# Kernel tuning notes

Hardware: AMD Instinct MI355X
Metric: run time of the kernel (lower is better)

## Reference

```python
import jax, jax.numpy as jnp
import numpy as np
from jax import lax

B, C_IN, T = 256, 1, 1632
HID, CB_DIM, NUM_TOK, NUM_Q = 64, 512, 1024, 2


def conv_k2s2(x, W, b):
    # Conv1d(kernel=2, stride=2): x [B,Ci,T] -> [B,Co,T//2]; W [Co,Ci,2]
    Bx, Ci, Tx = x.shape
    xr = x.reshape(Bx, Ci, Tx // 2, 2)
    return jnp.einsum('bitk,oik->bot', xr, W) + b[None, :, None]


def convT_k2s2(x, W, b):
    # ConvTranspose1d(kernel=2, stride=2): x [B,Ci,T] -> [B,Co,2T]; W [Ci,Co,2] (torch layout)
    Bx, Ci, Tx = x.shape
    y = jnp.einsum('bit,iok->botk', x, W)  # [B,Co,T,2]
    Co = W.shape[1]
    return y.reshape(Bx, Co, 2 * Tx) + b[None, :, None]


def conv1x1(x, W, b):
    # W [Co,Ci]
    return jnp.einsum('bit,oi->bot', x, W) + b[None, :, None]


def residual_vq(x, codebooks):
    # x [B,t,D]; codebooks [NUM_Q, NUM_TOK, D]. Euclidean argmin + straight-through.
    residual = x
    quantized_out = jnp.zeros_like(x)
    all_idx, all_loss = [], []
    for q in range(codebooks.shape[0]):
        cb = codebooks[q]  # [N,D]
        # squared euclidean distance, single large GEMM
        d2 = (jnp.sum(residual ** 2, -1, keepdims=True)
              - 2.0 * jnp.einsum('btd,nd->btn', residual, cb)
              + jnp.sum(cb ** 2, -1))  # [B,t,N]
        idx = jnp.argmin(d2, axis=-1)  # [B,t]
        quant = cb[idx]  # gather [B,t,D]
        # commitment loss (codebook treated as fixed / EMA-updated)
        loss = jnp.mean((lax.stop_gradient(quant) - residual) ** 2)
        # straight-through estimator
        quant_st = residual + lax.stop_gradient(quant - residual)
        residual = residual - lax.stop_gradient(quant)
        quantized_out = quantized_out + quant_st
        all_idx.append(idx)
        all_loss.append(loss)
    return quantized_out, jnp.stack(all_idx, -1), jnp.stack(all_loss)


def setup_inputs() -> dict:
    key = jax.random.key(0)
    ks = jax.random.split(key, 16)
    s = 0.02
    return {
        'img': jax.random.normal(ks[0], (B, C_IN, T), jnp.float32),
        'W_e1': jax.random.normal(ks[1], (HID, C_IN, 2), jnp.float32) * s,
        'b_e1': jnp.zeros((HID,), jnp.float32),
        'W_e2': jax.random.normal(ks[2], (HID, HID, 2), jnp.float32) * s,
        'b_e2': jnp.zeros((HID,), jnp.float32),
        'W_e3': jax.random.normal(ks[3], (CB_DIM, HID), jnp.float32) * s,
        'b_e3': jnp.zeros((CB_DIM,), jnp.float32),
        'codebooks': jax.random.normal(ks[4], (NUM_Q, NUM_TOK, CB_DIM), jnp.float32),
        'Wt_d1': jax.random.normal(ks[5], (CB_DIM, HID, 2), jnp.float32) * s,
        'b_d1': jnp.zeros((HID,), jnp.float32),
        'Wt_d2': jax.random.normal(ks[6], (HID, HID, 2), jnp.float32) * s,
        'b_d2': jnp.zeros((HID,), jnp.float32),
        'W_d3': jax.random.normal(ks[7], (C_IN, HID), jnp.float32) * s,
        'b_d3': jnp.zeros((C_IN,), jnp.float32),
    }


def reference(img, W_e1, b_e1, W_e2, b_e2, W_e3, b_e3, codebooks,
              Wt_d1, b_d1, Wt_d2, b_d2, W_d3, b_d3):
    # encoder
    h = jax.nn.relu(conv_k2s2(img, W_e1, b_e1))
    h = jax.nn.relu(conv_k2s2(h, W_e2, b_e2))
    encoded = conv1x1(h, W_e3, b_e3)  # [B,512,408]
    # residual VQ over tokens
    x = jnp.transpose(encoded, (0, 2, 1))  # b c t -> b t c
    quantized, indices, commit_loss = residual_vq(x, codebooks)
    quantized = jnp.transpose(quantized, (0, 2, 1))  # b t c -> b c t
    # decoder
    d = jax.nn.relu(convT_k2s2(quantized, Wt_d1, b_d1))
    d = jax.nn.relu(convT_k2s2(d, Wt_d2, b_d2))
    out = conv1x1(d, W_d3, b_d3)  # [B,1,1632]
    recon_loss = jnp.mean((img - out) ** 2)
    return out, recon_loss, commit_loss, indices, quantized
```

## Files before the change

### kernel.cpp

```cpp
#include <hip/hip_runtime.h>

#define NB    256
#define TLEN  1632
#define HIDC  64
#define CBD   512
#define NTOK  1024
#define T2L   816
#define T4L   408
#define MTOK  (NB*T4L)
#define M2TOK (NB*T2L)
#define MOUT  (NB*TLEN)

#define DO_OUT    ((size_t)0)
#define DO_RECON  ((size_t)417792)
#define DO_IDX    ((size_t)417795)
#define DO_QUANT  ((size_t)626691)

typedef unsigned short u16;
typedef unsigned long long u64;
typedef __attribute__((ext_vector_type(8))) short short8;
typedef __attribute__((ext_vector_type(4))) float f32x4;
typedef __attribute__((ext_vector_type(8))) _Float16 half8;
typedef __attribute__((ext_vector_type(4))) _Float16 half4;

static constexpr size_t OFF_XR  = 0;
static constexpr size_t OFF_H1  = OFF_XR + (size_t)MTOK*512;
static constexpr size_t OFF_H2  = OFF_H1 + (size_t)NB*T2L*64;
static constexpr size_t OFF_BE2 = OFF_H2 + (size_t)NB*T4L*64;
static constexpr size_t OFF_BD1 = OFF_BE2 + 8192;
static constexpr size_t OFF_BD2 = OFF_BD1 + 65536;
static constexpr size_t OFF_BX1 = OFF_BD2 + 8192;
static constexpr size_t OFF_BX2 = OFF_BX1 + 128;
static constexpr size_t OFF_ZB  = OFF_BX2 + 128;
static constexpr size_t OFF_C2  = OFF_ZB + 128;
static constexpr size_t OFF_SLOT= OFF_C2 + 2048;
static constexpr size_t OFF_IDXI= OFF_SLOT + 1536;
static constexpr size_t OFF_KEYS= OFF_IDXI + (size_t)MTOK*2;
static constexpr size_t OFF_FC  = OFF_KEYS + (size_t)MTOK*4;
static constexpr size_t OFF_FLAG= OFF_FC + 4;
static constexpr size_t OFF_CBH = OFF_FLAG + (size_t)MTOK*2;
static constexpr size_t OFF_CBL = OFF_CBH + 524288;
static constexpr size_t OFF_P0  = OFF_CBL + 524288;
static constexpr size_t OFF_P1  = OFF_P0 + 131072;

__device__ inline u64 shfl_xor_u64_w16(u64 v, int m) {
    unsigned lo = (unsigned)v, hi = (unsigned)(v >> 32);
    lo = __shfl_xor(lo, m, 16);
    hi = __shfl_xor(hi, m, 16);
    return (((u64)hi) << 32) | lo;
}
__device__ inline u64 packkey(float d, int n) {
    unsigned u = __float_as_uint(d);
    u = (u & 0x80000000u) ? ~u : (u | 0x80000000u);
    return (((u64)u) << 32) | (unsigned)n;
}
__device__ inline float unpackd(u64 k) {
    unsigned u = (unsigned)(k >> 32);
    u = (u & 0x80000000u) ? (u & 0x7fffffffu) : ~u;
    return __uint_as_float(u);
}
__device__ inline void merge2(u64& k1, u64& k2, u64 o1, u64 o2) {
    u64 n1 = (k1 < o1) ? k1 : o1;
    u64 hi = (k1 < o1) ? o1 : k1;
    u64 cand = (k1 <= o1) ? k2 : o2;
    u64 n2 = (hi < cand) ? hi : cand;
    k1 = n1; k2 = n2;
}
__device__ inline half4 cvt_h4(float4 v) {
    half4 h;
    h.x = (_Float16)v.x; h.y = (_Float16)v.y;
    h.z = (_Float16)v.z; h.w = (_Float16)v.w;
    return h;
}
__device__ inline half8 cvt_h8(float4 v0, float4 v1) {
    half8 h;
    h[0] = (_Float16)v0.x; h[1] = (_Float16)v0.y;
    h[2] = (_Float16)v0.z; h[3] = (_Float16)v0.w;
    h[4] = (_Float16)v1.x; h[5] = (_Float16)v1.y;
    h[6] = (_Float16)v1.z; h[7] = (_Float16)v1.w;
    return h;
}

__global__ void setup_kernel(const float* __restrict__ We2, const float* __restrict__ Wtd1,
                             const float* __restrict__ Wtd2, const float* __restrict__ bd1,
                             const float* __restrict__ bd2, const float* __restrict__ cbs,
                             float* __restrict__ Be2, float* __restrict__ Bd1,
                             float* __restrict__ Bd2, float* __restrict__ bx1, float* __restrict__ bx2,
                             u16* __restrict__ cbh, float* __restrict__ c2) {
    size_t t = (size_t)blockIdx.x * 256 + threadIdx.x;
    {
        float4 v = *(const float4*)(cbs + t * 4);
        *(half4*)&cbh[t * 4] = cvt_h4(v);
    }
    {
        int w = (int)(t >> 6);
        int lane = threadIdx.x & 63;
        if (w < 2048) {
            const float* r = cbs + (size_t)w * 512;
            float4 a = *(const float4*)(r + lane * 8);
            float4 b = *(const float4*)(r + lane * 8 + 4);
            float s = a.x*a.x + a.y*a.y + a.z*a.z + a.w*a.w + b.x*b.x + b.y*b.y + b.z*b.z + b.w*b.w;
            #pragma unroll
            for (int o = 32; o > 0; o >>= 1) s += __shfl_down(s, o, 64);
            if (lane == 0) c2[w] = s;
        }
    }
    size_t stride = (size_t)gridDim.x * 256;
    for (size_t x = t; x < 64 * 128; x += stride) {
        int c = (int)(x >> 7), k = (int)(x & 127);
        Be2[x] = We2[c * 128 + ((k & 63) << 1) + (k >> 6)];
    }
    for (size_t x = t; x < 128 * 512; x += stride) {
        int n = (int)(x >> 9), k = (int)(x & 511);
        Bd1[x] = Wtd1[k * 128 + n];
    }
    for (size_t x = t; x < 128 * 64; x += stride) {
        int n = (int)(x >> 6), k = (int)(x & 63);
        Bd2[x] = Wtd2[k * 128 + n];
    }
    for (size_t x = t; x < 128; x += stride) { bx1[x] = bd1[x >> 1]; bx2[x] = bd2[x >> 1]; }
}

__global__ void enc1_kernel(const float* __restrict__ img, const float* __restrict__ W,
                            const float* __restrict__ bias, float* __restrict__ h1) {
    int idx = blockIdx.x * 256 + threadIdx.x;
    int c = idx & 63;
    int t = (idx >> 6) % T2L;
    int b = idx / (64 * T2L);
    float v = W[c * 2] * img[(size_t)b * TLEN + 2 * t] +
              W[c * 2 + 1] * img[(size_t)b * TLEN + 2 * t + 1] + bias[c];
    h1[idx] = fmaxf(v, 0.f);
}

__global__ __launch_bounds__(256) void gemm_nt(const float* __restrict__ A, const float* __restrict__ Bw,
                        const float* __restrict__ bias, float* __restrict__ C,
                        int M, int N, int K, int amode, int relu) {
    __shared__ float As[32][132];
    __shared__ float Bs[32][68];
    int m0 = blockIdx.x * 128;
    int n0 = blockIdx.y * 64;
    int tid = threadIdx.x;
    int tx = tid & 15;
    int ty = tid >> 4;
    float acc[8][4];
    #pragma unroll
    for (int i = 0; i < 8; ++i)
        #pragma unroll
        for (int j = 0; j < 4; ++j) acc[i][j] = 0.f;

    for (int k0 = 0; k0 < K; k0 += 32) {
        #pragma unroll
        for (int i = 0; i < 4; ++i) {
            int idx = tid + i * 256;
            int row = idx >> 3;
            int kq = idx & 7;
            int m = m0 + row;
            size_t base;
            if (amode == 0) base = (size_t)m * K;
            else            base = (size_t)(((m / T4L) * T2L + 2 * (m % T4L)) * 64);
            float4 v = *(const float4*)(A + base + k0 + kq * 4);
            int kk = kq * 4;
            As[kk + 0][row] = v.x; As[kk + 1][row] = v.y;
            As[kk + 2][row] = v.z; As[kk + 3][row] = v.w;
        }
        #pragma unroll
        for (int i = 0; i < 2; ++i) {
            int idx = tid + i * 256;
            int row = idx >> 3;
            int kq = idx & 7;
            float4 v = *(const float4*)(Bw + (size_t)(n0 + row) * K + k0 + kq * 4);
            int kk = kq * 4;
            Bs[kk + 0][row] = v.x; Bs[kk + 1][row] = v.y;
            Bs[kk + 2][row] = v.z; Bs[kk + 3][row] = v.w;
        }
        __syncthreads();
        #pragma unroll
        for (int kk = 0; kk < 32; ++kk) {
            float a[8], bf[4];
            float4 a0 = *(const float4*)&As[kk][ty * 8];
            float4 a1 = *(const float4*)&As[kk][ty * 8 + 4];
            a[0]=a0.x; a[1]=a0.y; a[2]=a0.z; a[3]=a0.w;
            a[4]=a1.x; a[5]=a1.y; a[6]=a1.z; a[7]=a1.w;
            float4 b0 = *(const float4*)&Bs[kk][tx * 4];
            bf[0]=b0.x; bf[1]=b0.y; bf[2]=b0.z; bf[3]=b0.w;
            #pragma unroll
            for (int i = 0; i < 8; ++i)
                #pragma unroll
                for (int j = 0; j < 4; ++j) acc[i][j] += a[i] * bf[j];
        }
        __syncthreads();
    }
    #pragma unroll
    for (int i = 0; i < 8; ++i) {
        int m = m0 + ty * 8 + i;
        float4 v;
        v.x = acc[i][0] + bias[n0 + tx * 4 + 0];
        v.y = acc[i][1] + bias[n0 + tx * 4 + 1];
        v.z = acc[i][2] + bias[n0 + tx * 4 + 2];
        v.w = acc[i][3] + bias[n0 + tx * 4 + 3];
        if (relu) { v.x=fmaxf(v.x,0.f); v.y=fmaxf(v.y,0.f); v.z=fmaxf(v.z,0.f); v.w=fmaxf(v.w,0.f); }
        *(float4*)(C + (size_t)m * N + n0 + tx * 4) = v;
    }
}

template<int Q1>
__global__ __launch_bounds__(256, 3) void vq_f16_db(
    const float* __restrict__ Ap, const u16* __restrict__ cbh,
    const float* __restrict__ c2, const u64* __restrict__ prevkeys,
    const u16* __restrict__ cb0h, u64* __restrict__ pairs)
{
    __shared__ __align__(16) u16 As[2][128 * 40];
    __shared__ __align__(16) u16 Bs[2][128 * 40];
    int tid = threadIdx.x;
    int n0 = blockIdx.x * 128, m0 = blockIdx.y * 128;
    int lane = tid & 63, wid = tid >> 6;
    int lm = lane & 15, quad = lane >> 4;
    int wm = wid >> 1, wn = wid & 1;

    f32x4 acc[4][4];
    #pragma unroll
    for (int i = 0; i < 4; ++i)
        #pragma unroll
        for (int j = 0; j < 4; ++j) acc[i][j] = (f32x4){0.f, 0.f, 0.f, 0.f};

    int rw[2], cq[2];
    size_t coff[2];
    #pragma unroll
    for (int i = 0; i < 2; ++i) {
        int idx = tid + i * 256;
        rw[i] = idx >> 2; cq[i] = idx & 3;
        if (Q1) {
            int i0 = (int)(prevkeys[m0 + rw[i]] & 0xFFFFFFFFull);
            coff[i] = (size_t)i0 * 512;
        }
    }

#define VQ_LOAD(K0, AV0, AV1, CH, BV)                                                 \
    _Pragma("unroll")                                                                 \
    for (int i = 0; i < 2; ++i) {                                                     \
        AV0[i] = *(const float4*)(Ap + (size_t)(m0 + rw[i]) * 512 + (K0) + cq[i]*8);  \
        AV1[i] = *(const float4*)(Ap + (size_t)(m0 + rw[i]) * 512 + (K0) + cq[i]*8 + 4);\
        if (Q1) CH[i] = *(const half8*)(cb0h + coff[i] + (K0) + cq[i]*8);             \
        BV[i] = *(const short8*)(cbh + (size_t)(n0 + rw[i]) * 512 + (K0) + cq[i]*8);  \
    }

#define VQ_WRITE(BUF, AV0, AV1, CH, BV)                                               \
    _Pragma("unroll")                                                                 \
    for (int i = 0; i < 2; ++i) {                                                     \
        half8 hv = cvt_h8(AV0[i], AV1[i]);                                            \
        if (Q1) hv = hv - CH[i];                                                      \
        *(half8*)&As[BUF][rw[i] * 40 + cq[i] * 8] = hv;                               \
        *(short8*)&Bs[BUF][rw[i] * 40 + cq[i] * 8] = BV[i];                           \
    }

#define VQ_COMPUTE(BUF) {                                                             \
        half8 ah[4];                                                                  \
        _Pragma("unroll")                                                             \
        for (int mt = 0; mt < 4; ++mt)                                                \
            ah[mt] = *(const half8*)&As[BUF][(wm*64 + mt*16 + lm) * 40 + quad * 8];   \
        _Pragma("unroll")                                                             \
        for (int nt = 0; nt < 4; ++nt) {                                              \
            half8 bh = *(const half8*)&Bs[BUF][(wn*64 + nt*16 + lm) * 40 + quad * 8]; \
            _Pragma("unroll")                                                         \
            for (int mt = 0; mt < 4; ++mt)                                            \
                acc[mt][nt] = __builtin_amdgcn_mfma_f32_16x16x32_f16(ah[mt], bh, acc[mt][nt], 0, 0, 0); \
        }                                                                             \
    }

    float4 a0A[2], a1A[2], a0B[2], a1B[2];
    half8 chA[2], chB[2];
    short8 bvA[2], bvB[2];
    (void)chA; (void)chB;

    VQ_LOAD(0, a0A, a1A, chA, bvA);
    VQ_WRITE(0, a0A, a1A, chA, bvA);
    VQ_LOAD(32, a0B, a1B, chB, bvB);
    __syncthreads();

    for (int tp = 0; tp < 8; ++tp) {
        {
            VQ_WRITE(1, a0B, a1B, chB, bvB);
            if (tp < 7) { int K0 = (2 * tp + 2) * 32; VQ_LOAD(K0, a0A, a1A, chA, bvA); }
            VQ_COMPUTE(0);
            __syncthreads();
        }
        {
            if (tp < 7) { VQ_WRITE(0, a0A, a1A, chA, bvA); }
            if (tp < 7) { int K0 = (2 * tp + 3) * 32; VQ_LOAD(K0, a0B, a1B, chB, bvB); }
            VQ_COMPUTE(1);
            __syncthreads();
        }
    }
#undef VQ_LOAD
#undef VQ_WRITE
#undef VQ_COMPUTE

    float c2v[4];
    #pragma unroll
    for (int nt = 0; nt < 4; ++nt) c2v[nt] = c2[n0 + wn * 64 + nt * 16 + lm];

    u64* scr = (u64*)&As[0][0];
    #pragma unroll
    for (int mt = 0; mt < 4; ++mt) {
        #pragma unroll
        for (int rg = 0; rg < 4; ++rg) {
            int tl = wm * 64 + mt * 16 + quad * 4 + rg;
            u64 k1 = ~0ull, k2 = ~0ull;
            #pragma unroll
            for (int nt = 0; nt < 4; ++nt) {
                float d = c2v[nt] - 2.0f * acc[mt][nt][rg];
                u64 k = packkey(d, n0 + wn * 64 + nt * 16 + lm);
                if (k < k1) { k2 = k1; k1 = k; } else if (k < k2) { k2 = k; }
            }
            #pragma unroll
            for (int s = 1; s < 16; s <<= 1) {
                u64 o1 = shfl_xor_u64_w16(k1, s);
                u64 o2 = shfl_xor_u64_w16(k2, s);
                merge2(k1, k2, o1, o2);
            }
            if (lm == 0) { scr[wn * 256 + tl * 2] = k1; scr[wn * 256 + tl * 2 + 1] = k2; }
        }
    }
    __syncthreads();
    if (tid < 128) {
        u64 a1 = scr[tid * 2], a2 = scr[tid * 2 + 1];
        merge2(a1, a2, scr[256 + tid * 2], scr[256 + tid * 2 + 1]);
        size_t base = (size_t)(m0 + tid) * 16 + blockIdx.x * 2;
        pairs[base] = a1; pairs[base + 1] = a2;
    }
}

__global__ void vq_reduce(const u64* __restrict__ pairs, u64* __restrict__ keybuf,
                          int* __restrict__ fc, int* __restrict__ flaglist, float tau) {
    int m = blockIdx.x * 256 + threadIdx.x;
    const u64* p = pairs + (size_t)m * 16;
    u64 k1 = ~0ull, k2 = ~0ull;
    #pragma unroll
    for (int i = 0; i < 16; ++i) {
        u64 k = p[i];
        if (k < k1) { k2 = k1; k1 = k; } else if (k < k2) { k2 = k; }
    }
    keybuf[m] = k1;
    if (unpackd(k2) - unpackd(k1) < tau) {
        int pos = atomicAdd(fc, 1);
        flaglist[pos] = m;
    }
}

__global__ void vq_rescue(const float* __restrict__ xr, const float* __restrict__ cb,
                          const float* __restrict__ c2, const float* __restrict__ cb0,
                          const u64* __restrict__ prevkeys,
                          const int* __restrict__ fc, const int* __restrict__ flaglist,
                          u64* __restrict__ keybuf) {
    __shared__ u64 red[4];
    int cnt = *fc;
    int lane = threadIdx.x & 63, wid = threadIdx.x >> 6;
    for (int f = blockIdx.x; f < cnt; f += gridDim.x) {
        int m = flaglist[f];
        float4 rv0 = *(const float4*)(xr + (size_t)m * 512 + lane * 8);
        float4 rv1 = *(const float4*)(xr + (size_t)m * 512 + lane * 8 + 4);
        if (cb0) {
            size_t co = (size_t)(prevkeys[m] & 0xFFFFFFFFull) * 512;
            float4 c0 = *(const float4*)(cb0 + co + lane * 8);
            float4 c1 = *(const float4*)(cb0 + co + lane * 8 + 4);
            rv0.x -= c0.x; rv0.y -= c0.y; rv0.z -= c0.z; rv0.w -= c0.w;
            rv1.x -= c1.x; rv1.y -= c1.y; rv1.z -= c1.z; rv1.w -= c1.w;
        }
        u64 best = ~0ull;
        for (int c = wid * 256; c < wid * 256 + 256; ++c) {
            const float* cp = cb + (size_t)c * 512 + lane * 8;
            float4 c0 = *(const float4*)cp;
            float4 c1 = *(const float4*)(cp + 4);
            float p = rv0.x*c0.x + rv0.y*c0.y + rv0.z*c0.z + rv0.w*c0.w
                    + rv1.x*c1.x + rv1.y*c1.y + rv1.z*c1.z + rv1.w*c1.w;
            #pragma unroll
            for (int s = 1; s < 64; s <<= 1) p += __shfl_xor(p, s, 64);
            u64 k = packkey(c2[c] - 2.0f * p, c);
            if (k < best) best = k;
        }
        if (lane == 0) red[wid] = best;
        __syncthreads();
        if (threadIdx.x == 0) {
            u64 b = red[0];
            if (red[1] < b) b = red[1];
            if (red[2] < b) b = red[2];
            if (red[3] < b) b = red[3];
            keybuf[m] = b;
        }
        __syncthreads();
    }
}

__global__ void commit_idx_kernel(const float* __restrict__ xr,
                                  const float* __restrict__ cb0f, const float* __restrict__ cb1f,
                                  const u64* __restrict__ keys0, const u64* __restrict__ keys1,
                                  float* __restrict__ idx_f, int* __restrict__ idx_i,
                                  float* __restrict__ slots) {
    int tid = threadIdx.x;
    int lane = tid & 63;
    int m = blockIdx.x * 4 + (tid >> 6);
    unsigned i0 = (unsigned)(keys0[m] & 0xFFFFFFFFull);
    unsigned i1 = (unsigned)(keys1[m] & 0xFFFFFFFFull);
    const float* x = xr + (size_t)m * 512 + lane * 8;
    const float* c0 = cb0f + (size_t)i0 * 512 + lane * 8;
    const float* c1 = cb1f + (size_t)i1 * 512 + lane * 8;
    float4 x0 = *(const float4*)x, x1 = *(const float4*)(x + 4);
    float4 a0 = *(const float4*)c0, a1 = *(const float4*)(c0 + 4);
    float4 b0 = *(const float4*)c1, b1 = *(const float4*)(c1 + 4);
    x0.x -= a0.x; x0.y -= a0.y; x0.z -= a0.z; x0.w -= a0.w;
    x1.x -= a1.x; x1.y -= a1.y; x1.z -= a1.z; x1.w -= a1.w;
    float s1 = x0.x*x0.x + x0.y*x0.y + x0.z*x0.z + x0.w*x0.w
             + x1.x*x1.x + x1.y*x1.y + x1.z*x1.z + x1.w*x1.w;
    x0.x -= b0.x; x0.y -= b0.y; x0.z -= b0.z; x0.w -= b0.w;
    x1.x -= b1.x; x1.y -= b1.y; x1.z -= b1.z; x1.w -= b1.w;
    float s2 = x0.x*x0.x + x0.y*x0.y + x0.z*x0.z + x0.w*x0.w
             + x1.x*x1.x + x1.y*x1.y + x1.z*x1.z + x1.w*x1.w;
    #pragma unroll
    for (int o = 32; o > 0; o >>= 1) { s1 += __shfl_down(s1, o, 64); s2 += __shfl_down(s2, o, 64); }
    if (lane == 0) {
        atomicAdd(&slots[512 + (m & 511)], s1);
        atomicAdd(&slots[1024 + (m & 511)], s2);
        idx_f[(size_t)m * 2]     = (float)i0;
        idx_f[(size_t)m * 2 + 1] = (float)i1;
        idx_i[m * 2] = (int)i0;
        idx_i[m * 2 + 1] = (int)i1;
    }
}

__global__ void quant_out_kernel(const float* __restrict__ cb0, const float* __restrict__ cb1,
                                 const int* __restrict__ idxi, float* __restrict__ out4) {
    __shared__ float buf[64][129];
    __shared__ int i0s[64], i1s[64];
    int b = blockIdx.x;
    int t0 = blockIdx.y * 64;
    int c0 = blockIdx.z * 128;
    int tid = threadIdx.x;
    if (tid < 64) {
        int t = t0 + tid;
        int i0 = 0, i1 = 0;
        if (t < T4L) { i0 = idxi[(b * T4L + t) * 2]; i1 = idxi[(b * T4L + t) * 2 + 1]; }
        i0s[tid] = i0; i1s[tid] = i1;
    }
    __syncthreads();
    int cl = tid & 127, th = tid >> 7;
    for (int t = th; t < 64; t += 2) {
        if (t0 + t < T4L)
            buf[t][cl] = cb0[(size_t)i0s[t] * 512 + c0 + cl] + cb1[(size_t)i1s[t] * 512 + c0 + cl];
    }
    __syncthreads();
    int lane = tid & 63, ch = tid >> 6;
    for (int cc = ch; cc < 128; cc += 4) {
        int t = t0 + lane;
        if (t < T4L) out4[((size_t)b * 512 + c0 + cc) * T4L + t] = buf[lane][cc];
    }
}

__global__ void d1_gather_kernel(const float* __restrict__ P0, const float* __restrict__ P1,
                                 const int* __restrict__ idxi, const float* __restrict__ bx1,
                                 float* __restrict__ d1) {
    int x = blockIdx.x * 256 + threadIdx.x;
    int n = x & 127;
    int m = x >> 7;
    int b = m / T4L, t = m % T4L;
    int i0 = idxi[m * 2], i1 = idxi[m * 2 + 1];
    float v = P0[i0 * 128 + n] + P1[i1 * 128 + n] + bx1[n];
    v = fmaxf(v, 0.f);
    d1[((size_t)(b * T2L + 2 * t + (n & 1))) * 64 + (n >> 1)] = v;
}

__global__ __launch_bounds__(256) void dec2_fused(
    const float* __restrict__ d1, const float* __restrict__ Bd2, const float* __restrict__ bx2,
    const float* __restrict__ W3, const float* __restrict__ b3, const float* __restrict__ img,
    float* __restrict__ out, float* __restrict__ slots)
{
    __shared__ float As[32][132];
    __shared__ float Bs[32][132];
    __shared__ float w3s[64];
    int m0 = blockIdx.x * 128;
    int tid = threadIdx.x;
    int tx = tid & 15;
    int ty = tid >> 4;
    if (tid < 64) w3s[tid] = W3[tid];
    float acc[8][8];
    #pragma unroll
    for (int i = 0; i < 8; ++i)
        #pragma unroll
        for (int j = 0; j < 8; ++j) acc[i][j] = 0.f;

    for (int k0 = 0; k0 < 64; k0 += 32) {
        #pragma unroll
        for (int i = 0; i < 4; ++i) {
            int idx = tid + i * 256;
            int row = idx >> 3;
            int kq = idx & 7;
            float4 v = *(const float4*)(d1 + (size_t)(m0 + row) * 64 + k0 + kq * 4);
            int kk = kq * 4;
            As[kk + 0][row] = v.x; As[kk + 1][row] = v.y;
            As[kk + 2][row] = v.z; As[kk + 3][row] = v.w;
        }
        #pragma unroll
        for (int i = 0; i < 4; ++i) {
            int idx = tid + i * 256;
            int row = idx >> 3;
            int kq = idx & 7;
            float4 v = *(const float4*)(Bd2 + (size_t)row * 64 + k0 + kq * 4);
            int kk = kq * 4;
            Bs[kk + 0][row] = v.x; Bs[kk + 1][row] = v.y;
            Bs[kk + 2][row] = v.z; Bs[kk + 3][row] = v.w;
        }
        __syncthreads();
        #pragma unroll
        for (int kk = 0; kk < 32; ++kk) {
            float a[8], bf[8];
            float4 a0 = *(const float4*)&As[kk][ty * 8];
            float4 a1 = *(const float4*)&As[kk][ty * 8 + 4];
            a[0]=a0.x; a[1]=a0.y; a[2]=a0.z; a[3]=a0.w;
            a[4]=a1.x; a[5]=a1.y; a[6]=a1.z; a[7]=a1.w;
            float4 b0 = *(const float4*)&Bs[kk][tx * 4];
            float4 b1 = *(const float4*)&Bs[kk][64 + tx * 4];
            bf[0]=b0.x; bf[1]=b0.y; bf[2]=b0.z; bf[3]=b0.w;
            bf[4]=b1.x; bf[5]=b1.y; bf[6]=b1.z; bf[7]=b1.w;
            #pragma unroll
            for (int i = 0; i < 8; ++i)
                #pragma unroll
                for (int j = 0; j < 8; ++j) acc[i][j] += a[i] * bf[j];
        }
        __syncthreads();
    }
    float bb3 = b3[0];
    float local = 0.f;
    #pragma unroll
    for (int i = 0; i < 8; ++i) {
        float s0 = 0.f, s1 = 0.f;
        #pragma unroll
        for (int j = 0; j < 4; ++j) {
            int n = tx * 4 + j;
            float v = fmaxf(acc[i][j] + bx2[n], 0.f);
            float w = w3s[n >> 1];
            if (j & 1) s1 += w * v; else s0 += w * v;
            int n2 = 64 + tx * 4 + j;
            float v2 = fmaxf(acc[i][j + 4] + bx2[n2], 0.f);
            float w2 = w3s[n2 >> 1];
            if (j & 1) s1 += w2 * v2; else s0 += w2 * v2;
        }
        #pragma unroll
        for (int o = 8; o > 0; o >>= 1) { s0 += __shfl_down(s0, o, 16); s1 += __shfl_down(s1, o, 16); }
        if (tx == 0) {
            int m = m0 + ty * 8 + i;
            int b = m / T2L, t2 = m % T2L;
            size_t o0 = (size_t)b * TLEN + 2 * t2;
            float v0 = s0 + bb3, v1 = s1 + bb3;
            out[o0] = v0; out[o0 + 1] = v1;
            float e0 = img[o0] - v0, e1 = img[o0 + 1] - v1;
            local += e0 * e0 + e1 * e1;
        }
    }
    if (tx == 0) atomicAdd(&slots[(blockIdx.x * 16 + ty) & 511], local);
}

__global__ void finalize_kernel(const float* __restrict__ slots, float* __restrict__ out_scalars) {
    __shared__ float red[256];
    int tid = threadIdx.x;
    for (int which = 0; which < 3; ++which) {
        float s = slots[which * 512 + tid] + slots[which * 512 + tid + 256];
        red[tid] = s; __syncthreads();
        for (int st = 128; st > 0; st >>= 1) { if (tid < st) red[tid] += red[tid + st]; __syncthreads(); }
        if (tid == 0) {
            float denom = (which == 0) ? (float)MOUT : (float)((size_t)MTOK * 512);
            out_scalars[which] = red[0] / denom;
        }
        __syncthreads();
    }
}

extern "C" void kernel_launch(void* const* d_in, const int* in_sizes, int n_in,
                              void* d_out, int out_size, void* d_ws, size_t ws_size,
                              hipStream_t stream) {
    const float* img  = (const float*)d_in[0];
    const float* We1  = (const float*)d_in[1];
    const float* be1  = (const float*)d_in[2];
    const float* We2  = (const float*)d_in[3];
    const float* be2  = (const float*)d_in[4];
    const float* We3  = (const float*)d_in[5];
    const float* be3  = (const float*)d_in[6];
    const float* cbs  = (const float*)d_in[7];
    const float* Wtd1 = (const float*)d_in[8];
    const float* bd1  = (const float*)d_in[9];
    const float* Wtd2 = (const float*)d_in[10];
    const float* bd2  = (const float*)d_in[11];
    const float* Wd3  = (const float*)d_in[12];
    const float* bd3  = (const float*)d_in[13];

    float* w = (float*)d_ws;
    float* xr   = w + OFF_XR;
    float* h1   = w + OFF_H1;
    float* h2   = w + OFF_H2;
    float* Be2  = w + OFF_BE2;
    float* Bd1  = w + OFF_BD1;
    float* Bd2  = w + OFF_BD2;
    float* bx1  = w + OFF_BX1;
    float* bx2  = w + OFF_BX2;
    float* zerob= w + OFF_ZB;
    float* c2   = w + OFF_C2;
    float* slots= w + OFF_SLOT;
    int*   idxi = (int*)(w + OFF_IDXI);
    u64*   keys = (u64*)(w + OFF_KEYS);
    int*   fc   = (int*)(w + OFF_FC);
    int*   flag = (int*)(w + OFF_FLAG);
    u16*   cbh  = (u16*)(w + OFF_CBH);
    float* P0   = w + OFF_P0;
    float* P1   = w + OFF_P1;
    u64*   pairs= (u64*)(w + OFF_H2);

    float* outp = (float*)d_out;
    float* out0   = outp + DO_OUT;
    float* oscal  = outp + DO_RECON;
    float* idxf   = outp + DO_IDX;
    float* qout   = outp + DO_QUANT;

    hipMemsetAsync(slots, 0, 1536 * sizeof(float), stream);
    hipMemsetAsync(fc, 0, 2 * sizeof(int), stream);
    hipMemsetAsync(zerob, 0, 128 * sizeof(float), stream);

    setup_kernel<<<1024, 256, 0, stream>>>(We2, Wtd1, Wtd2, bd1, bd2, cbs,
                                           Be2, Bd1, Bd2, bx1, bx2, cbh, c2);

    const float* cb1p = cbs + (size_t)NTOK * CBD;

    gemm_nt<<<dim3(8, 2), 256, 0, stream>>>(cbs,  Bd1, zerob, P0, 1024, 128, 512, 0, 0);
    gemm_nt<<<dim3(8, 2), 256, 0, stream>>>(cb1p, Bd1, zerob, P1, 1024, 128, 512, 0, 0);

    enc1_kernel<<<(NB * T2L * HIDC) / 256, 256, 0, stream>>>(img, We1, be1, h1);
    gemm_nt<<<dim3(MTOK / 128, 1), 256, 0, stream>>>(h1, Be2, be2, h2, MTOK, 64, 128, 1, 1);
    gemm_nt<<<dim3(MTOK / 128, 8), 256, 0, stream>>>(h2, We3, be3, xr, MTOK, 512, 64, 0, 0);

    vq_f16_db<0><<<dim3(8, MTOK / 128), 256, 0, stream>>>(xr, cbh, c2, nullptr, nullptr, pairs);
    vq_reduce<<<MTOK / 256, 256, 0, stream>>>(pairs, keys, fc + 0, flag, 0.05f);
    vq_rescue<<<1024, 256, 0, stream>>>(xr, cbs, c2, nullptr, nullptr, fc + 0, flag, keys);
    vq_f16_db<1><<<dim3(8, MTOK / 128), 256, 0, stream>>>(xr, cbh + (size_t)NTOK * 512,
                                                          c2 + NTOK, keys, cbh, pairs);
    vq_reduce<<<MTOK / 256, 256, 0, stream>>>(pairs, keys + MTOK, fc + 1, flag + MTOK, 0.15f);
    vq_rescue<<<1024, 256, 0, stream>>>(xr, cb1p, c2 + NTOK, cbs, keys, fc + 1, flag + MTOK, keys + MTOK);

    commit_idx_kernel<<<MTOK / 4, 256, 0, stream>>>(xr, cbs, cb1p, keys, keys + MTOK, idxf, idxi, slots);

    quant_out_kernel<<<dim3(NB, 7, 4), 256, 0, stream>>>(cbs, cb1p, idxi, qout);

    d1_gather_kernel<<<(MTOK * 128) / 256, 256, 0, stream>>>(P0, P1, idxi, bx1, h1);
    dec2_fused<<<M2TOK / 128, 256, 0, stream>>>(h1, Bd2, bx2, Wd3, bd3, img, out0, slots);

    finalize_kernel<<<1, 256, 0, stream>>>(slots, oscal);
}
```

Measured before the change: 1.319 ms.

## Widen VQ distance GEMM tile to 256 codes with direct-to-LDS codebook loads

Each block of the VQ distance kernel now covers 256 codebook entries instead of 128. This halves the grid in N and halves how often each fp32 activation tile is reloaded and converted. The codebook tile is copied straight from global memory into LDS with global_load_lds, using an XOR-swizzled layout to avoid bank conflicts, which saves register staging. The pairs buffer moves to its own workspace region and the reduce reads 8 partial candidates per token instead of 16. The costs are twice the accumulator registers and occupancy dropping from 3 to 2 waves per SIMD.

```diff
diff --git a/kernel.cpp b/kernel.cpp
--- a/kernel.cpp
+++ b/kernel.cpp
@@ -42,6 +42,7 @@
 static constexpr size_t OFF_CBL = OFF_CBH + 524288;
 static constexpr size_t OFF_P0  = OFF_CBL + 524288;
 static constexpr size_t OFF_P1  = OFF_P0 + 131072;
+static constexpr size_t OFF_PAIRS = OFF_P1 + 131072;
 
 __device__ inline u64 shfl_xor_u64_w16(u64 v, int m) {
     unsigned lo = (unsigned)v, hi = (unsigned)(v >> 32);
@@ -79,6 +80,10 @@
     h[4] = (_Float16)v1.x; h[5] = (_Float16)v1.y;
     h[6] = (_Float16)v1.z; h[7] = (_Float16)v1.w;
     return h;
+}
+__device__ inline void gll16(const u16* g, u16* l) {
+    __builtin_amdgcn_global_load_lds((const __attribute__((address_space(1))) void*)g,
+                                     (__attribute__((address_space(3))) void*)l, 16, 0, 0);
 }
 
 __global__ void setup_kernel(const float* __restrict__ We2, const float* __restrict__ Wtd1,
@@ -204,53 +209,62 @@
 }
 
 template<int Q1>
-__global__ __launch_bounds__(256, 3) void vq_f16_db(
+__global__ __launch_bounds__(256, 2) void vq_f16_db(
     const float* __restrict__ Ap, const u16* __restrict__ cbh,
     const float* __restrict__ c2, const u64* __restrict__ prevkeys,
     const u16* __restrict__ cb0h, u64* __restrict__ pairs)
 {
     __shared__ __align__(16) u16 As[2][128 * 40];
-    __shared__ __align__(16) u16 Bs[2][128 * 40];
+    __shared__ __align__(16) u16 Bs[2][256 * 32];
     int tid = threadIdx.x;
-    int n0 = blockIdx.x * 128, m0 = blockIdx.y * 128;
+    int n0 = blockIdx.x * 256, m0 = blockIdx.y * 128;
     int lane = tid & 63, wid = tid >> 6;
     int lm = lane & 15, quad = lane >> 4;
     int wm = wid >> 1, wn = wid & 1;
 
-    f32x4 acc[4][4];
+    f32x4 acc[4][8];
     #pragma unroll
     for (int i = 0; i < 4; ++i)
         #pragma unroll
-        for (int j = 0; j < 4; ++j) acc[i][j] = (f32x4){0.f, 0.f, 0.f, 0.f};
-
-    int rw[2], cq[2];
-    size_t coff[2];
+        for (int j = 0; j < 8; ++j) acc[i][j] = (f32x4){0.f, 0.f, 0.f, 0.f};
+
+    int ar[2], acq[2], coffA[2];
     #pragma unroll
     for (int i = 0; i < 2; ++i) {
         int idx = tid + i * 256;
-        rw[i] = idx >> 2; cq[i] = idx & 3;
-        if (Q1) {
-            int i0 = (int)(prevkeys[m0 + rw[i]] & 0xFFFFFFFFull);
-            coff[i] = (size_t)i0 * 512;
-        }
-    }
-
-#define VQ_LOAD(K0, AV0, AV1, CH, BV)                                                 \
+        ar[i] = idx >> 2; acq[i] = idx & 3;
+        coffA[i] = 0;
+        if (Q1) coffA[i] = (int)(prevkeys[m0 + ar[i]] & 0xFFFFFFFFull) * 512;
+    }
+    int brow[4], bchk[4];
+    #pragma unroll
+    for (int i = 0; i < 4; ++i) {
+        brow[i] = i * 64 + wid * 16 + (lane >> 2);
+        bchk[i] = (lane & 3) ^ ((brow[i] >> 1) & 3);
+    }
+
+#define VQ_GLLB(BUF, K0)                                                              \
+    _Pragma("unroll")                                                                 \
+    for (int i = 0; i < 4; ++i) {                                                     \
+        const u16* gp = cbh + (size_t)(n0 + brow[i]) * 512 + (K0) + bchk[i] * 8;      \
+        gll16(gp, &Bs[BUF][i * 2048 + wid * 512]);                                    \
+    }
+
+#define VQ_LOADA(K0, V0, V1, CH)                                                      \
     _Pragma("unroll")                                                                 \
     for (int i = 0; i < 2; ++i) {                                                     \
-        AV0[i] = *(const float4*)(Ap + (size_t)(m0 + rw[i]) * 512 + (K0) + cq[i]*8);  \
-        AV1[i] = *(const float4*)(Ap + (size_t)(m0 + rw[i]) * 512 + (K0) + cq[i]*8 + 4);\
-        if (Q1) CH[i] = *(const half8*)(cb0h + coff[i] + (K0) + cq[i]*8);             \
-        BV[i] = *(const short8*)(cbh + (size_t)(n0 + rw[i]) * 512 + (K0) + cq[i]*8);  \
-    }
-
-#define VQ_WRITE(BUF, AV0, AV1, CH, BV)                                               \
+        const float* s = Ap + (size_t)(m0 + ar[i]) * 512 + (K0) + acq[i] * 8;         \
+        V0[i] = *(const float4*)s;                                                    \
+        V1[i] = *(const float4*)(s + 4);                                              \
+        if (Q1) CH[i] = *(const half8*)(cb0h + coffA[i] + (K0) + acq[i] * 8);         \
+    }
+
+#define VQ_WRITEA(BUF, V0, V1, CH)                                                    \
     _Pragma("unroll")                                                                 \
     for (int i = 0; i < 2; ++i) {                                                     \
-        half8 hv = cvt_h8(AV0[i], AV1[i]);                                            \
+        half8 hv = cvt_h8(V0[i], V1[i]);                                              \
         if (Q1) hv = hv - CH[i];                                                      \
-        *(half8*)&As[BUF][rw[i] * 40 + cq[i] * 8] = hv;                               \
-        *(short8*)&Bs[BUF][rw[i] * 40 + cq[i] * 8] = BV[i];                           \
+        *(half8*)&As[BUF][ar[i] * 40 + acq[i] * 8] = hv;                              \
     }
 
 #define VQ_COMPUTE(BUF) {                                                             \
@@ -259,45 +273,51 @@
         for (int mt = 0; mt < 4; ++mt)                                                \
             ah[mt] = *(const half8*)&As[BUF][(wm*64 + mt*16 + lm) * 40 + quad * 8];   \
         _Pragma("unroll")                                                             \
-        for (int nt = 0; nt < 4; ++nt) {                                              \
-            half8 bh = *(const half8*)&Bs[BUF][(wn*64 + nt*16 + lm) * 40 + quad * 8]; \
+        for (int nt = 0; nt < 8; ++nt) {                                              \
+            int rn = wn * 128 + nt * 16 + lm;                                         \
+            half8 bh = *(const half8*)&Bs[BUF][rn * 32 + ((quad ^ ((rn >> 1) & 3)) * 8)]; \
             _Pragma("unroll")                                                         \
             for (int mt = 0; mt < 4; ++mt)                                            \
                 acc[mt][nt] = __builtin_amdgcn_mfma_f32_16x16x32_f16(ah[mt], bh, acc[mt][nt], 0, 0, 0); \
         }                                                                             \
     }
 
-    float4 a0A[2], a1A[2], a0B[2], a1B[2];
+    float4 v0A[2], v1A[2], v0B[2], v1B[2];
     half8 chA[2], chB[2];
-    short8 bvA[2], bvB[2];
     (void)chA; (void)chB;
 
-    VQ_LOAD(0, a0A, a1A, chA, bvA);
-    VQ_WRITE(0, a0A, a1A, chA, bvA);
-    VQ_LOAD(32, a0B, a1B, chB, bvB);
+    VQ_GLLB(0, 0);
+    VQ_LOADA(0, v0A, v1A, chA);
+    VQ_WRITEA(0, v0A, v1A, chA);
+    VQ_LOADA(32, v0B, v1B, chB);
     __syncthreads();
 
     for (int tp = 0; tp < 8; ++tp) {
         {
-            VQ_WRITE(1, a0B, a1B, chB, bvB);
-            if (tp < 7) { int K0 = (2 * tp + 2) * 32; VQ_LOAD(K0, a0A, a1A, chA, bvA); }
+            VQ_GLLB(1, (2 * tp + 1) * 32);
+            VQ_WRITEA(1, v0B, v1B, chB);
+            if (tp < 7) { VQ_LOADA((2 * tp + 2) * 32, v0A, v1A, chA); }
             VQ_COMPUTE(0);
             __syncthreads();
         }
         {
-            if (tp < 7) { VQ_WRITE(0, a0A, a1A, chA, bvA); }
-            if (tp < 7) { int K0 = (2 * tp + 3) * 32; VQ_LOAD(K0, a0B, a1B, chB, bvB); }
+            if (tp < 7) {
+                VQ_GLLB(0, (2 * tp + 2) * 32);
+                VQ_WRITEA(0, v0A, v1A, chA);
+                VQ_LOADA((2 * tp + 3) * 32, v0B, v1B, chB);
+            }
             VQ_COMPUTE(1);
             __syncthreads();
         }
     }
-#undef VQ_LOAD
-#undef VQ_WRITE
+#undef VQ_GLLB
+#undef VQ_LOADA
+#undef VQ_WRITEA
 #undef VQ_COMPUTE
 
-    float c2v[4];
-    #pragma unroll
-    for (int nt = 0; nt < 4; ++nt) c2v[nt] = c2[n0 + wn * 64 + nt * 16 + lm];
+    float c2v[8];
+    #pragma unroll
+    for (int nt = 0; nt < 8; ++nt) c2v[nt] = c2[n0 + wn * 128 + nt * 16 + lm];
 
     u64* scr = (u64*)&As[0][0];
     #pragma unroll
@@ -307,9 +327,9 @@
             int tl = wm * 64 + mt * 16 + quad * 4 + rg;
             u64 k1 = ~0ull, k2 = ~0ull;
             #pragma unroll
-            for (int nt = 0; nt < 4; ++nt) {
+            for (int nt = 0; nt < 8; ++nt) {
                 float d = c2v[nt] - 2.0f * acc[mt][nt][rg];
-                u64 k = packkey(d, n0 + wn * 64 + nt * 16 + lm);
+                u64 k = packkey(d, n0 + wn * 128 + nt * 16 + lm);
                 if (k < k1) { k2 = k1; k1 = k; } else if (k < k2) { k2 = k; }
             }
             #pragma unroll
@@ -325,7 +345,7 @@
     if (tid < 128) {
         u64 a1 = scr[tid * 2], a2 = scr[tid * 2 + 1];
         merge2(a1, a2, scr[256 + tid * 2], scr[256 + tid * 2 + 1]);
-        size_t base = (size_t)(m0 + tid) * 16 + blockIdx.x * 2;
+        size_t base = (size_t)(m0 + tid) * 8 + blockIdx.x * 2;
         pairs[base] = a1; pairs[base + 1] = a2;
     }
 }
@@ -333,10 +353,10 @@
 __global__ void vq_reduce(const u64* __restrict__ pairs, u64* __restrict__ keybuf,
                           int* __restrict__ fc, int* __restrict__ flaglist, float tau) {
     int m = blockIdx.x * 256 + threadIdx.x;
-    const u64* p = pairs + (size_t)m * 16;
+    const u64* p = pairs + (size_t)m * 8;
     u64 k1 = ~0ull, k2 = ~0ull;
     #pragma unroll
-    for (int i = 0; i < 16; ++i) {
+    for (int i = 0; i < 8; ++i) {
         u64 k = p[i];
         if (k < k1) { k2 = k1; k1 = k; } else if (k < k2) { k2 = k; }
     }
@@ -610,7 +630,7 @@
     u16*   cbh  = (u16*)(w + OFF_CBH);
     float* P0   = w + OFF_P0;
     float* P1   = w + OFF_P1;
-    u64*   pairs= (u64*)(w + OFF_H2);
+    u64*   pairs= (u64*)(w + OFF_PAIRS);
 
     float* outp = (float*)d_out;
     float* out0   = outp + DO_OUT;
@@ -634,10 +654,10 @@
     gemm_nt<<<dim3(MTOK / 128, 1), 256, 0, stream>>>(h1, Be2, be2, h2, MTOK, 64, 128, 1, 1);
     gemm_nt<<<dim3(MTOK / 128, 8), 256, 0, stream>>>(h2, We3, be3, xr, MTOK, 512, 64, 0, 0);
 
-    vq_f16_db<0><<<dim3(8, MTOK / 128), 256, 0, stream>>>(xr, cbh, c2, nullptr, nullptr, pairs);
+    vq_f16_db<0><<<dim3(4, MTOK / 128), 256, 0, stream>>>(xr, cbh, c2, nullptr, nullptr, pairs);
     vq_reduce<<<MTOK / 256, 256, 0, stream>>>(pairs, keys, fc + 0, flag, 0.05f);
     vq_rescue<<<1024, 256, 0, stream>>>(xr, cbs, c2, nullptr, nullptr, fc + 0, flag, keys);
-    vq_f16_db<1><<<dim3(8, MTOK / 128), 256, 0, stream>>>(xr, cbh + (size_t)NTOK * 512,
+    vq_f16_db<1><<<dim3(4, MTOK / 128), 256, 0, stream>>>(xr, cbh + (size_t)NTOK * 512,
                                                           c2 + NTOK, keys, cbh, pairs);
     vq_reduce<<<MTOK / 256, 256, 0, stream>>>(pairs, keys + MTOK, fc + 1, flag + MTOK, 0.15f);
     vq_rescue<<<1024, 256, 0, stream>>>(xr, cb1p, c2 + NTOK, cbs, keys, fc + 1, flag + MTOK, keys + MTOK);
```

New measurement: 1.163 ms. -11.8%, faster.
